# Kernel optimization log

Measured on AMD Instinct MI355X. Metric: run time of the kernel, lower is better.

## Reference

```python
import jax, jax.numpy as jnp
import numpy as np

H = 1024   # hidden_size
A = 16     # num_actions
T = 64     # time steps
N = 128    # batch (parallel envs)


def setup_inputs() -> dict:
    key = jax.random.key(0)
    ks = jax.random.split(key, 16)
    s = 0.02  # small-ish init scale for weights
    a_idx = jax.random.randint(ks[5], (T, N), 0, A)
    return {
        "x": jax.random.normal(ks[0], (T * N, H), jnp.float32),
        "hxs_gru": jax.random.normal(ks[1], (N, H), jnp.float32),
        "hxs_p": jax.random.normal(ks[2], (N, 2 * H), jnp.float32),
        # masks are 0/1 episode-reset flags
        "masks": jax.random.bernoulli(ks[3], 0.95, (T * N, 1)).astype(jnp.float32),
        "prev_action_one_hot": jax.nn.one_hot(a_idx, A, dtype=jnp.float32),
        "w_ih": jax.random.normal(ks[6], (3 * H, H), jnp.float32) * s,
        "w_hh": jax.random.normal(ks[7], (3 * H, H), jnp.float32) * s,
        "b_ih": jnp.zeros((3 * H,), jnp.float32),
        "b_hh": jnp.zeros((3 * H,), jnp.float32),
        "p_w1": jax.random.normal(ks[8], (2 * H, 2 * H + A), jnp.float32) * s,
        "p_b1": jnp.zeros((2 * H,), jnp.float32),
        "p_w2": jax.random.normal(ks[9], (H, 2 * H), jnp.float32) * s,
        "p_b2": jnp.zeros((H,), jnp.float32),
        "mu_w": jax.random.normal(ks[10], (H, H), jnp.float32) * s,
        "mu_b": jnp.zeros((H,), jnp.float32),
        "lv_w": jax.random.normal(ks[11], (H, H), jnp.float32) * s,
        "lv_b": jnp.zeros((H,), jnp.float32),
    }


def reference(x, hxs_gru, hxs_p, masks, prev_action_one_hot,
              w_ih, w_hh, b_ih, b_hh,
              p_w1, p_b1, p_w2, p_b2,
              mu_w, mu_b, lv_w, lv_b):
    n = hxs_gru.shape[0]
    h_dim = hxs_gru.shape[1]
    t = x.shape[0] // n
    xT = x.reshape(t, n, h_dim)        # [T,N,H]
    mT = masks.reshape(t, n, 1)        # [T,N,1]

    # ---- _forward_gru: masked GRUCell recurrence over time ----
    def gru_step(h, inp):
        x_t, m_t = inp
        h0 = h * m_t                                  # per-step state reset
        gi = x_t @ w_ih.T + b_ih                      # [N,3H]
        gh = h0 @ w_hh.T + b_hh                       # [N,3H]
        ir, iz, inn = jnp.split(gi, 3, axis=1)
        hr, hz, hn = jnp.split(gh, 3, axis=1)
        r = jax.nn.sigmoid(ir + hr)
        z = jax.nn.sigmoid(iz + hz)
        nn_ = jnp.tanh(inn + r * hn)
        h_new = (1.0 - z) * nn_ + z * h0              # PyTorch GRUCell update
        return h_new, h_new

    gru_hxs, gru_acc = jax.lax.scan(gru_step, hxs_gru, (xT, mT))
    gru_acc = gru_acc.reshape(t * n, h_dim)

    # ---- _forward_p_gru: MLP recurrence with mask-gated state/action ----
    def p_step(h, inp):
        x_t, m_t, a_t = inp
        hidden = h * m_t + jnp.concatenate([x_t, x_t], axis=1) * (1.0 - m_t)
        cur = jnp.concatenate([a_t * m_t, hidden], axis=1)   # [N, A+2H]
        d = jax.nn.relu(cur @ p_w1.T + p_b1)                 # [N, 2H]
        d = jax.nn.relu(d @ p_w2.T + p_b2)                   # [N, H]
        mu = d @ mu_w.T + mu_b                               # [N, H]
        lv = d @ lv_w.T + lv_b                               # [N, H]
        h_new = jnp.concatenate([mu, x_t], axis=1)           # [N, 2H]
        return h_new, (mu, lv)

    # note: original concatenates action first: cat((a*m, hidden))
    p_hxs, (p_mu, p_lv) = jax.lax.scan(p_step, hxs_p, (xT, mT, prev_action_one_hot))
    p_mu = p_mu.reshape(t * n, h_dim)
    p_lv = p_lv.reshape(t * n, h_dim)
    return (gru_acc, gru_hxs, p_mu, p_lv, p_hxs)
```

## Files before the change

kernel.cpp:

```cpp
#include <hip/hip_runtime.h>

typedef unsigned int uint;
typedef unsigned short ushort;
typedef __bf16 bf16x8_t __attribute__((ext_vector_type(8)));
typedef float f32x4_t __attribute__((ext_vector_type(4)));

__device__ __forceinline__ ushort f2b(float f) {
    uint u = __builtin_bit_cast(uint, f);
    u += 0x7fffu + ((u >> 16) & 1u);
    return (ushort)(u >> 16);
}
__device__ __forceinline__ float b2f(ushort h) {
    return __builtin_bit_cast(float, (uint)h << 16);
}
__device__ __forceinline__ float sigm(float v) { return 1.f / (1.f + __expf(-v)); }
__device__ __forceinline__ float tanh_(float v) {
    v = fmaxf(-15.f, fminf(15.f, v));
    float e = __expf(2.f * v);
    return (e - 1.f) / (e + 1.f);
}

__device__ __forceinline__ uint ld_cg_u32(const uint* p) {
    uint r;
    asm volatile("global_load_dword %0, %1, off sc0 sc1\n\ts_waitcnt vmcnt(0)"
                 : "=v"(r) : "v"(p) : "memory");
    return r;
}
__device__ __forceinline__ void st_cg_u32(uint* p, uint v) {
    asm volatile("global_store_dword %0, %1, off sc0 sc1" :: "v"(p), "v"(v) : "memory");
}
__device__ __forceinline__ void st_cg_u16(ushort* p, uint v) {
    asm volatile("global_store_short %0, %1, off sc0 sc1" :: "v"(p), "v"(v) : "memory");
}
__device__ __forceinline__ void ld8_nw(uint4 u[8],
    const void* p0, const void* p1, const void* p2, const void* p3,
    const void* p4, const void* p5, const void* p6, const void* p7)
{
    asm volatile(
        "global_load_dwordx4 %0, %8, off sc0 sc1\n\t"
        "global_load_dwordx4 %1, %9, off sc0 sc1\n\t"
        "global_load_dwordx4 %2, %10, off sc0 sc1\n\t"
        "global_load_dwordx4 %3, %11, off sc0 sc1\n\t"
        "global_load_dwordx4 %4, %12, off sc0 sc1\n\t"
        "global_load_dwordx4 %5, %13, off sc0 sc1\n\t"
        "global_load_dwordx4 %6, %14, off sc0 sc1\n\t"
        "global_load_dwordx4 %7, %15, off sc0 sc1"
        : "=&v"(u[0]), "=&v"(u[1]), "=&v"(u[2]), "=&v"(u[3]),
          "=&v"(u[4]), "=&v"(u[5]), "=&v"(u[6]), "=&v"(u[7])
        : "v"(p0), "v"(p1), "v"(p2), "v"(p3), "v"(p4), "v"(p5), "v"(p6), "v"(p7)
        : "memory");
}
__device__ __forceinline__ void vm0() {
    asm volatile("s_waitcnt vmcnt(0)" ::: "memory");
    __builtin_amdgcn_sched_barrier(0);
}
__device__ __forceinline__ bf16x8_t u2b(uint4 u) { return __builtin_bit_cast(bf16x8_t, u); }

#define SMEM_BYTES 36864
union U8 { ushort h[8]; uint4 v; };

template<int BN, int EPI, bool AF32>
__device__ __forceinline__ void gemm_body(
    int bx, int by, const void* Av, int lda,
    const ushort* Bp, int ldb, int K,
    void* Ov, int ldo, const float* bias, char* smem)
{
    constexpr int LDW = 72;
    ushort* As = (ushort*)smem;
    ushort* Bs = (ushort*)(smem + 128 * LDW * 2);
    const int tid = threadIdx.x, lane = tid & 63, wid = tid >> 6;
    constexpr int WC = (BN == 128) ? 2 : 1;
    constexpr int WR = 4 / WC;
    constexpr int WROWS = 128 / WR;
    constexpr int WCOLS = BN / WC;
    constexpr int MI = WROWS / 16, NI = WCOLS / 16;
    const int wr = (WC == 2) ? (wid >> 1) : wid;
    const int wc = (WC == 2) ? (wid & 1) : 0;
    const int row0 = by * 128, col0 = bx * BN;

    f32x4_t acc[MI][NI];
#pragma unroll
    for (int i = 0; i < MI; i++)
#pragma unroll
        for (int j = 0; j < NI; j++) acc[i][j] = (f32x4_t){0.f, 0.f, 0.f, 0.f};

    for (int k0 = 0; k0 < K; k0 += 64) {
        __syncthreads();
#pragma unroll
        for (int cc = 0; cc < 4; cc++) {
            int chunk = tid + cc * 256;
            int r = chunk >> 3, c8 = chunk & 7;
            uint4 val;
            if constexpr (AF32) {
                const float* Af = (const float*)Av + (size_t)(row0 + r) * lda + k0 + c8 * 8;
                float4 v0 = ((const float4*)Af)[0];
                float4 v1 = ((const float4*)Af)[1];
                U8 u;
                u.h[0] = f2b(v0.x); u.h[1] = f2b(v0.y); u.h[2] = f2b(v0.z); u.h[3] = f2b(v0.w);
                u.h[4] = f2b(v1.x); u.h[5] = f2b(v1.y); u.h[6] = f2b(v1.z); u.h[7] = f2b(v1.w);
                val = u.v;
            } else {
                val = *(const uint4*)((const ushort*)Av + (size_t)(row0 + r) * lda + k0 + c8 * 8);
            }
            *(uint4*)&As[r * LDW + c8 * 8] = val;
        }
#pragma unroll
        for (int cc = 0; cc < BN / 32; cc++) {
            int chunk = tid + cc * 256;
            int r = chunk >> 3, c8 = chunk & 7;
            uint4 val = *(const uint4*)(Bp + (size_t)(col0 + r) * ldb + k0 + c8 * 8);
            *(uint4*)&Bs[r * LDW + c8 * 8] = val;
        }
        __syncthreads();
#pragma unroll
        for (int kk = 0; kk < 64; kk += 32) {
            int ko = kk + ((lane >> 4) << 3);
            bf16x8_t af[MI], bf[NI];
#pragma unroll
            for (int mi = 0; mi < MI; mi++)
                af[mi] = *(const bf16x8_t*)&As[(wr * WROWS + mi * 16 + (lane & 15)) * LDW + ko];
#pragma unroll
            for (int ni = 0; ni < NI; ni++)
                bf[ni] = *(const bf16x8_t*)&Bs[(wc * WCOLS + ni * 16 + (lane & 15)) * LDW + ko];
#pragma unroll
            for (int mi = 0; mi < MI; mi++)
#pragma unroll
                for (int ni = 0; ni < NI; ni++)
                    acc[mi][ni] = __builtin_amdgcn_mfma_f32_16x16x32_bf16(af[mi], bf[ni], acc[mi][ni], 0, 0, 0);
        }
    }
#pragma unroll
    for (int mi = 0; mi < MI; mi++) {
#pragma unroll
        for (int ni = 0; ni < NI; ni++) {
            int gcol = col0 + wc * WCOLS + ni * 16 + (lane & 15);
#pragma unroll
            for (int i = 0; i < 4; i++) {
                int grow = row0 + wr * WROWS + mi * 16 + ((lane >> 4) << 2) + i;
                float v = acc[mi][ni][i];
                if constexpr (EPI == 0) {
                    ((float*)Ov)[(size_t)grow * ldo + gcol] = v + bias[gcol];
                } else if constexpr (EPI == 1) {
                    ((ushort*)Ov)[(size_t)grow * ldo + gcol] = f2b(v);
                } else {
                    ((ushort*)Ov)[(size_t)grow * ldo + gcol] = f2b(v + bias[gcol]);
                }
            }
        }
    }
}

template<int BN, int EPI, bool AF32>
__global__ __launch_bounds__(256) void gemm_k(
    const void* A, int lda, const ushort* B, int ldb, int K,
    void* O, int ldo, const float* bias)
{
    __shared__ char smem[SMEM_BYTES];
    gemm_body<BN, EPI, AF32>(blockIdx.x, blockIdx.y, A, lda, B, ldb, K, O, ldo, bias, smem);
}

#define NFLAG_G 0
#define NFLAG_A 4096
#define NFLAG_B 12288
#define NFLAGS  20480

__device__ __forceinline__ void wg_wait(uint* f, int n, int tid) {
    if (tid < n) {
        while (ld_cg_u32(f + tid) == 0u) __builtin_amdgcn_s_sleep(1);
    }
    __syncthreads();
}

__device__ __forceinline__ void wg_arrive(uint* slot, int tid) {
    __syncthreads();
    if (tid == 0) st_cg_u32(slot, 1u);
}

__device__ void role_gru(int cb, const ushort* __restrict__ whhb, ushort* hb,
                         const ushort* __restrict__ gi, const float* masks,
                         const float* b_ih, const float* b_hh, const float* hxs_g,
                         float* out, uint* flags, char* lds)
{
    const int tid = threadIdx.x, lane = tid & 63, w = tid >> 6;
    const int colL = cb * 16 + (lane & 15);
    const int kw = w * 256;
    const int kl = (lane >> 4) << 3;

    bf16x8_t bw[3][8];
#pragma unroll
    for (int g = 0; g < 3; g++)
#pragma unroll
        for (int ks = 0; ks < 8; ks++)
            bw[g][ks] = *(const bf16x8_t*)(whhb + (size_t)(g * 1024 + colL) * 1024 + kw + ks * 32 + kl);

    const float bihr = b_ih[colL], bihz = b_ih[1024 + colL], bihn = b_ih[2048 + colL];
    const float bhhr = b_hh[colL], bhhz = b_hh[1024 + colL], bhhn = b_hh[2048 + colL];

    f32x4_t hown[2];
#pragma unroll
    for (int j = 0; j < 2; j++)
#pragma unroll
        for (int i = 0; i < 4; i++)
            hown[j][i] = hxs_g[(size_t)((2 * w + j) * 16 + ((lane >> 4) << 2) + i) * 1024 + colL];

    for (int t = 0; t < 64; t++) {
        if (t) wg_wait(flags + NFLAG_G + (t - 1) * 64, 64, tid);
        float mc[2][4], mn[2][4], g0p[2][4], g1p[2][4], g2p[2][4];
#pragma unroll
        for (int j = 0; j < 2; j++) {
            const int rt = 2 * w + j;
#pragma unroll
            for (int i = 0; i < 4; i++) {
                const int row = rt * 16 + ((lane >> 4) << 2) + i;
                mc[j][i] = masks[t * 128 + row];
                mn[j][i] = (t < 63) ? masks[(t + 1) * 128 + row] : 0.f;
                const size_t gib = (size_t)(t * 128 + row) * 3072;
                g0p[j][i] = b2f(gi[gib + colL]);
                g1p[j][i] = b2f(gi[gib + 1024 + colL]);
                g2p[j][i] = b2f(gi[gib + 2048 + colL]);
            }
        }
        const ushort* A = hb + (size_t)(t & 1) * 131072;
        const ushort* base = A + (size_t)(lane & 15) * 1024 + kw + kl;
        f32x4_t acc[3][8];
#pragma unroll
        for (int g = 0; g < 3; g++)
#pragma unroll
            for (int rt = 0; rt < 8; rt++) acc[g][rt] = (f32x4_t){0.f, 0.f, 0.f, 0.f};
#pragma unroll
        for (int half = 0; half < 2; half++) {
            const ushort* b = base + half * 128;
            uint4 u0[8], u1[8], u2[8], u3[8];
            ld8_nw(u0, b, b + 16384, b + 32768, b + 49152, b + 65536, b + 81920, b + 98304, b + 114688);
            ld8_nw(u1, b + 32, b + 16384 + 32, b + 32768 + 32, b + 49152 + 32, b + 65536 + 32, b + 81920 + 32, b + 98304 + 32, b + 114688 + 32);
            ld8_nw(u2, b + 64, b + 16384 + 64, b + 32768 + 64, b + 49152 + 64, b + 65536 + 64, b + 81920 + 64, b + 98304 + 64, b + 114688 + 64);
            ld8_nw(u3, b + 96, b + 16384 + 96, b + 32768 + 96, b + 49152 + 96, b + 65536 + 96, b + 81920 + 96, b + 98304 + 96, b + 114688 + 96);
            vm0();
#pragma unroll
            for (int g = 0; g < 3; g++)
#pragma unroll
                for (int rt = 0; rt < 8; rt++) {
                    acc[g][rt] = __builtin_amdgcn_mfma_f32_16x16x32_bf16(u2b(u0[rt]), bw[g][half * 4 + 0], acc[g][rt], 0, 0, 0);
                    acc[g][rt] = __builtin_amdgcn_mfma_f32_16x16x32_bf16(u2b(u1[rt]), bw[g][half * 4 + 1], acc[g][rt], 0, 0, 0);
                    acc[g][rt] = __builtin_amdgcn_mfma_f32_16x16x32_bf16(u2b(u2[rt]), bw[g][half * 4 + 2], acc[g][rt], 0, 0, 0);
                    acc[g][rt] = __builtin_amdgcn_mfma_f32_16x16x32_bf16(u2b(u3[rt]), bw[g][half * 4 + 3], acc[g][rt], 0, 0, 0);
                }
        }
#pragma unroll
        for (int g = 0; g < 3; g++)
#pragma unroll
            for (int rt = 0; rt < 8; rt++)
                *(f32x4_t*)(lds + ((size_t)(w * 24 + g * 8 + rt) * 64 + lane) * 16) = acc[g][rt];
        __syncthreads();
#pragma unroll
        for (int j = 0; j < 2; j++) {
            const int rt = 2 * w + j;
            f32x4_t sg[3];
#pragma unroll
            for (int g = 0; g < 3; g++) {
                sg[g] = (f32x4_t){0.f, 0.f, 0.f, 0.f};
#pragma unroll
                for (int ww = 0; ww < 4; ww++)
                    sg[g] += *(const f32x4_t*)(lds + ((size_t)(ww * 24 + g * 8 + rt) * 64 + lane) * 16);
            }
#pragma unroll
            for (int i = 0; i < 4; i++) {
                const int row = rt * 16 + ((lane >> 4) << 2) + i;
                const float h0 = hown[j][i] * mc[j][i];
                const float rv = sigm(g0p[j][i] + bihr + bhhr + sg[0][i]);
                const float zv = sigm(g1p[j][i] + bihz + bhhz + sg[1][i]);
                const float nv = tanh_(g2p[j][i] + bihn + rv * (sg[2][i] + bhhn));
                const float hnew = (1.f - zv) * nv + zv * h0;
                out[(size_t)(t * 128 + row) * 1024 + colL] = hnew;
                hown[j][i] = hnew;
                if (t < 63)
                    st_cg_u16(hb + (size_t)((t + 1) & 1) * 131072 + (size_t)row * 1024 + colL,
                              (uint)f2b(hnew * mn[j][i]));
            }
        }
        wg_arrive(flags + NFLAG_G + t * 64 + cb, tid);
    }
}

__device__ void role_p(int p, const ushort* __restrict__ Wcb, const ushort* __restrict__ w1h1b,
                       const ushort* __restrict__ hp1b, const ushort* __restrict__ w2b,
                       const ushort* __restrict__ d1pre, const float* masks, const float* cvec,
                       const float* p_b2, ushort* d1r, ushort* d2r, uint* flags, char* lds)
{
    const int tid = threadIdx.x, lane = tid & 63, w = tid >> 6;
    const int rowg = p >> 6, colg = p & 63;
    const int rA0 = rowg * 64, cA0 = colg * 32;
    const int rB0 = rowg * 64, cB0 = colg * 16;
    const int kwA = w * 256, kwB = w * 512, kl = (lane >> 4) << 3;

    bf16x8_t wcF[2][8];
#pragma unroll
    for (int ct = 0; ct < 2; ct++)
#pragma unroll
        for (int ks = 0; ks < 8; ks++)
            wcF[ct][ks] = *(const bf16x8_t*)(Wcb + (size_t)(cA0 + ct * 16 + (lane & 15)) * 1024 + kwA + ks * 32 + kl);
    bf16x8_t w2F[16];
#pragma unroll
    for (int ks = 0; ks < 16; ks++)
        w2F[ks] = *(const bf16x8_t*)(w2b + (size_t)(cB0 + (lane & 15)) * 2048 + kwB + ks * 32 + kl);
    const float cv0 = cvec[cA0 + (lane & 15)], cv1 = cvec[cA0 + 16 + (lane & 15)];
    const float pb = p_b2[cB0 + (lane & 15)];

    for (int t = 0; t < 64; t++) {
        if (t) wg_wait(flags + NFLAG_B + (t - 1) * 128 + rowg * 64, 64, tid);
        float mA[4], preA[2][4];
#pragma unroll
        for (int i = 0; i < 4; i++) {
            const int row = rA0 + w * 16 + ((lane >> 4) << 2) + i;
            mA[i] = masks[t * 128 + row];
            preA[0][i] = b2f(d1pre[(size_t)(t * 128 + row) * 2048 + cA0 + (lane & 15)]);
            preA[1][i] = b2f(d1pre[(size_t)(t * 128 + row) * 2048 + cA0 + 16 + (lane & 15)]);
        }
        f32x4_t accA[2][4];
#pragma unroll
        for (int ct = 0; ct < 2; ct++)
#pragma unroll
            for (int rt = 0; rt < 4; rt++) accA[ct][rt] = (f32x4_t){0.f, 0.f, 0.f, 0.f};
        if (t == 0) {
#pragma unroll
            for (int ks = 0; ks < 8; ks++) {
                bf16x8_t af[4], b0[2];
#pragma unroll
                for (int ct = 0; ct < 2; ct++)
                    b0[ct] = *(const bf16x8_t*)(w1h1b + (size_t)(cA0 + ct * 16 + (lane & 15)) * 1024 + kwA + ks * 32 + kl);
#pragma unroll
                for (int rt = 0; rt < 4; rt++)
                    af[rt] = *(const bf16x8_t*)(hp1b + (size_t)(rA0 + rt * 16 + (lane & 15)) * 1024 + kwA + ks * 32 + kl);
#pragma unroll
                for (int ct = 0; ct < 2; ct++)
#pragma unroll
                    for (int rt = 0; rt < 4; rt++)
                        accA[ct][rt] = __builtin_amdgcn_mfma_f32_16x16x32_bf16(af[rt], b0[ct], accA[ct][rt], 0, 0, 0);
            }
        } else {
            const ushort* Ab = d2r + (size_t)(t - 1) * 131072 + (size_t)(rA0 + (lane & 15)) * 1024 + kwA + kl;
            uint4 u0[8], u1[8], u2[8], u3[8];
            ld8_nw(u0, Ab,       Ab + 16384,       Ab + 32768,       Ab + 49152,       Ab + 32,  Ab + 16384 + 32,  Ab + 32768 + 32,  Ab + 49152 + 32);
            ld8_nw(u1, Ab + 64,  Ab + 16384 + 64,  Ab + 32768 + 64,  Ab + 49152 + 64,  Ab + 96,  Ab + 16384 + 96,  Ab + 32768 + 96,  Ab + 49152 + 96);
            ld8_nw(u2, Ab + 128, Ab + 16384 + 128, Ab + 32768 + 128, Ab + 49152 + 128, Ab + 160, Ab + 16384 + 160, Ab + 32768 + 160, Ab + 49152 + 160);
            ld8_nw(u3, Ab + 192, Ab + 16384 + 192, Ab + 32768 + 192, Ab + 49152 + 192, Ab + 224, Ab + 16384 + 224, Ab + 32768 + 224, Ab + 49152 + 224);
            vm0();
#pragma unroll
            for (int ct = 0; ct < 2; ct++)
#pragma unroll
                for (int rt = 0; rt < 4; rt++) {
                    accA[ct][rt] = __builtin_amdgcn_mfma_f32_16x16x32_bf16(u2b(u0[rt]), wcF[ct][0], accA[ct][rt], 0, 0, 0);
                    accA[ct][rt] = __builtin_amdgcn_mfma_f32_16x16x32_bf16(u2b(u0[4 + rt]), wcF[ct][1], accA[ct][rt], 0, 0, 0);
                    accA[ct][rt] = __builtin_amdgcn_mfma_f32_16x16x32_bf16(u2b(u1[rt]), wcF[ct][2], accA[ct][rt], 0, 0, 0);
                    accA[ct][rt] = __builtin_amdgcn_mfma_f32_16x16x32_bf16(u2b(u1[4 + rt]), wcF[ct][3], accA[ct][rt], 0, 0, 0);
                    accA[ct][rt] = __builtin_amdgcn_mfma_f32_16x16x32_bf16(u2b(u2[rt]), wcF[ct][4], accA[ct][rt], 0, 0, 0);
                    accA[ct][rt] = __builtin_amdgcn_mfma_f32_16x16x32_bf16(u2b(u2[4 + rt]), wcF[ct][5], accA[ct][rt], 0, 0, 0);
                    accA[ct][rt] = __builtin_amdgcn_mfma_f32_16x16x32_bf16(u2b(u3[rt]), wcF[ct][6], accA[ct][rt], 0, 0, 0);
                    accA[ct][rt] = __builtin_amdgcn_mfma_f32_16x16x32_bf16(u2b(u3[4 + rt]), wcF[ct][7], accA[ct][rt], 0, 0, 0);
                }
        }
#pragma unroll
        for (int ct = 0; ct < 2; ct++)
#pragma unroll
            for (int rt = 0; rt < 4; rt++)
                *(f32x4_t*)(lds + ((size_t)(w * 8 + ct * 4 + rt) * 64 + lane) * 16) = accA[ct][rt];
        __syncthreads();
#pragma unroll
        for (int ct = 0; ct < 2; ct++) {
            f32x4_t s = (f32x4_t){0.f, 0.f, 0.f, 0.f};
#pragma unroll
            for (int ww = 0; ww < 4; ww++)
                s += *(const f32x4_t*)(lds + ((size_t)(ww * 8 + ct * 4 + w) * 64 + lane) * 16);
            const int col = cA0 + ct * 16 + (lane & 15);
            const float cvt = (t == 0) ? 0.f : (ct ? cv1 : cv0);
#pragma unroll
            for (int i = 0; i < 4; i++) {
                const int row = rA0 + w * 16 + ((lane >> 4) << 2) + i;
                float f = preA[ct][i] + mA[i] * (s[i] + cvt);
                st_cg_u16(d1r + (size_t)row * 2048 + col, (uint)f2b(f > 0.f ? f : 0.f));
            }
        }
        wg_arrive(flags + NFLAG_A + t * 128 + p, tid);
        wg_wait(flags + NFLAG_A + t * 128 + rowg * 64, 64, tid);
        f32x4_t accB[4];
#pragma unroll
        for (int rt = 0; rt < 4; rt++) accB[rt] = (f32x4_t){0.f, 0.f, 0.f, 0.f};
        const ushort* Bb = d1r + (size_t)(rB0 + (lane & 15)) * 2048 + kwB + kl;
#pragma unroll
        for (int half = 0; half < 2; half++) {
            const ushort* b = Bb + half * 256;
            uint4 u0[8], u1[8], u2[8], u3[8];
            ld8_nw(u0, b,       b + 32768,       b + 65536,       b + 98304,       b + 32,  b + 32768 + 32,  b + 65536 + 32,  b + 98304 + 32);
            ld8_nw(u1, b + 64,  b + 32768 + 64,  b + 65536 + 64,  b + 98304 + 64,  b + 96,  b + 32768 + 96,  b + 65536 + 96,  b + 98304 + 96);
            ld8_nw(u2, b + 128, b + 32768 + 128, b + 65536 + 128, b + 98304 + 128, b + 160, b + 32768 + 160, b + 65536 + 160, b + 98304 + 160);
            ld8_nw(u3, b + 192, b + 32768 + 192, b + 65536 + 192, b + 98304 + 192, b + 224, b + 32768 + 224, b + 65536 + 224, b + 98304 + 224);
            vm0();
#pragma unroll
            for (int rt = 0; rt < 4; rt++) {
                accB[rt] = __builtin_amdgcn_mfma_f32_16x16x32_bf16(u2b(u0[rt]), w2F[half * 8 + 0], accB[rt], 0, 0, 0);
                accB[rt] = __builtin_amdgcn_mfma_f32_16x16x32_bf16(u2b(u0[4 + rt]), w2F[half * 8 + 1], accB[rt], 0, 0, 0);
                accB[rt] = __builtin_amdgcn_mfma_f32_16x16x32_bf16(u2b(u1[rt]), w2F[half * 8 + 2], accB[rt], 0, 0, 0);
                accB[rt] = __builtin_amdgcn_mfma_f32_16x16x32_bf16(u2b(u1[4 + rt]), w2F[half * 8 + 3], accB[rt], 0, 0, 0);
                accB[rt] = __builtin_amdgcn_mfma_f32_16x16x32_bf16(u2b(u2[rt]), w2F[half * 8 + 4], accB[rt], 0, 0, 0);
                accB[rt] = __builtin_amdgcn_mfma_f32_16x16x32_bf16(u2b(u2[4 + rt]), w2F[half * 8 + 5], accB[rt], 0, 0, 0);
                accB[rt] = __builtin_amdgcn_mfma_f32_16x16x32_bf16(u2b(u3[rt]), w2F[half * 8 + 6], accB[rt], 0, 0, 0);
                accB[rt] = __builtin_amdgcn_mfma_f32_16x16x32_bf16(u2b(u3[4 + rt]), w2F[half * 8 + 7], accB[rt], 0, 0, 0);
            }
        }
#pragma unroll
        for (int rt = 0; rt < 4; rt++)
            *(f32x4_t*)(lds + ((size_t)(w * 4 + rt) * 64 + lane) * 16) = accB[rt];
        __syncthreads();
        {
            f32x4_t s = (f32x4_t){0.f, 0.f, 0.f, 0.f};
#pragma unroll
            for (int ww = 0; ww < 4; ww++)
                s += *(const f32x4_t*)(lds + ((size_t)(ww * 4 + w) * 64 + lane) * 16);
            const int col = cB0 + (lane & 15);
#pragma unroll
            for (int i = 0; i < 4; i++) {
                const int row = rB0 + w * 16 + ((lane >> 4) << 2) + i;
                float f = s[i] + pb;
                st_cg_u16(d2r + (size_t)(t * 128 + row) * 1024 + col, (uint)f2b(f > 0.f ? f : 0.f));
            }
        }
        wg_arrive(flags + NFLAG_B + t * 128 + p, tid);
    }
}

__global__ __launch_bounds__(256, 1) void persist_k(
    const ushort* whhb, const ushort* Wcb, const ushort* w1h1b, const ushort* w2b,
    const ushort* gi, const ushort* d1pre, const ushort* hp1b,
    ushort* hb, ushort* d1r, ushort* d2r,
    const float* masks, const float* b_ih, const float* b_hh,
    const float* cvec, const float* p_b2, const float* hxs_g,
    float* out, uint* flags)
{
    __shared__ __align__(16) char lds[98304];
    const int wg = blockIdx.x;
    if (wg < 64) role_gru(wg, whhb, hb, gi, masks, b_ih, b_hh, hxs_g, out, flags, lds);
    else         role_p(wg - 64, Wcb, w1h1b, hp1b, w2b, d1pre, masks, cvec, p_b2, d1r, d2r, flags, lds);
}

__global__ void prep_w(const float* w_ih, const float* w_hh, const float* p_w1,
                       const float* p_w2, const float* mu_w, const float* lv_w,
                       ushort* wihb, ushort* whhb, ushort* w2b, ushort* muwb,
                       ushort* lvwb, ushort* muwTb, ushort* w1h1b, ushort* pw1b)
{
    const long total = 17956864;
    for (long idx = (long)blockIdx.x * 256 + threadIdx.x; idx < total; idx += (long)gridDim.x * 256) {
        long l = idx;
        if (l < 3145728) { wihb[l] = f2b(w_ih[l]); continue; } l -= 3145728;
        if (l < 3145728) { whhb[l] = f2b(w_hh[l]); continue; } l -= 3145728;
        if (l < 2097152) { w2b[l] = f2b(p_w2[l]); continue; } l -= 2097152;
        if (l < 1048576) { muwb[l] = f2b(mu_w[l]); continue; } l -= 1048576;
        if (l < 1048576) { lvwb[l] = f2b(lv_w[l]); continue; } l -= 1048576;
        if (l < 1048576) {
            int c = (int)(l >> 10), o = (int)(l & 1023);
            muwTb[l] = f2b(mu_w[(size_t)o * 1024 + c]); continue;
        } l -= 1048576;
        if (l < 2097152) {
            int r = (int)(l >> 10), c = (int)(l & 1023);
            w1h1b[l] = f2b(p_w1[(size_t)r * 2064 + 16 + c]); continue;
        } l -= 2097152;
        {
            int r = (int)(l / 2112), c = (int)(l - (long)r * 2112);
            pw1b[l] = (c < 2064) ? f2b(p_w1[(size_t)r * 2064 + c]) : (ushort)0;
        }
    }
}

__global__ void prep_x(const float* x, const float* hxs_g, const float* hxs_p,
                       const float* masks, const float* oh,
                       ushort* ain, ushort* hb0, ushort* hp1b)
{
    const long totA = 8192L * 2112, totH = 131072, totP = 131072;
    for (long idx = (long)blockIdx.x * 256 + threadIdx.x; idx < totA + totH + totP; idx += (long)gridDim.x * 256) {
        if (idx < totA) {
            long j = idx;
            int i = (int)(j / 2112);
            int c = (int)(j - (long)i * 2112);
            float m = masks[i];
            float v;
            if (c < 16) v = oh[(size_t)i * 16 + c] * m;
            else if (c < 1040) v = x[(size_t)i * 1024 + (c - 16)] * (1.f - m);
            else if (c < 2064) {
                int cc = c - 1040;
                float xp = (i >= 128) ? x[(size_t)(i - 128) * 1024 + cc]
                                      : hxs_p[(size_t)i * 2048 + 1024 + cc];
                v = xp * m + x[(size_t)i * 1024 + cc] * (1.f - m);
            } else v = 0.f;
            ain[j] = f2b(v);
            continue;
        }
        long j = idx - totA;
        if (j < totH) {
            int row = (int)(j >> 10), c = (int)(j & 1023);
            hb0[j] = f2b(hxs_g[(size_t)row * 1024 + c] * masks[row]);
            continue;
        }
        j -= totH;
        {
            int row = (int)(j >> 10), c = (int)(j & 1023);
            hp1b[j] = f2b(hxs_p[(size_t)row * 2048 + c]);
        }
    }
}

__global__ void k_cvec(const float* p_w1, const float* mu_b, float* cvec)
{
    int j = blockIdx.x * 4 + (threadIdx.x >> 6);
    int lane = threadIdx.x & 63;
    float s = 0.f;
    for (int o = lane; o < 1024; o += 64) s += p_w1[(size_t)j * 2064 + 16 + o] * mu_b[o];
#pragma unroll
    for (int off = 32; off; off >>= 1) s += __shfl_down(s, off);
    if (lane == 0) cvec[j] = s;
}

__global__ void init_flags(uint* flags)
{
    int i = blockIdx.x * 256 + threadIdx.x;
    if (i < NFLAGS) flags[i] = 0u;
}

__global__ void k_tail(float* out, const float* x)
{
    const long total = 131072 + 262144;
    for (long idx = (long)blockIdx.x * 256 + threadIdx.x; idx < total; idx += (long)gridDim.x * 256) {
        if (idx < 131072) {
            out[8388608 + idx] = out[8257536 + idx];
        } else {
            long j = idx - 131072;
            int n = (int)(j >> 11), c = (int)(j & 2047);
            out[25296896 + j] = (c < 1024)
                ? out[8519680 + (size_t)(8064 + n) * 1024 + c]
                : x[(size_t)(8064 + n) * 1024 + (c - 1024)];
        }
    }
}

extern "C" void kernel_launch(void* const* d_in, const int* in_sizes, int n_in,
                              void* d_out, int out_size, void* d_ws, size_t ws_size,
                              hipStream_t stream)
{
    (void)in_sizes; (void)n_in; (void)out_size; (void)ws_size;
    const float* x      = (const float*)d_in[0];
    const float* hxs_g  = (const float*)d_in[1];
    const float* hxs_p  = (const float*)d_in[2];
    const float* masks  = (const float*)d_in[3];
    const float* oh     = (const float*)d_in[4];
    const float* w_ih   = (const float*)d_in[5];
    const float* w_hh   = (const float*)d_in[6];
    const float* b_ih   = (const float*)d_in[7];
    const float* b_hh   = (const float*)d_in[8];
    const float* p_w1   = (const float*)d_in[9];
    const float* p_b1   = (const float*)d_in[10];
    const float* p_w2   = (const float*)d_in[11];
    const float* p_b2   = (const float*)d_in[12];
    const float* mu_w   = (const float*)d_in[13];
    const float* mu_b   = (const float*)d_in[14];
    const float* lv_w   = (const float*)d_in[15];
    const float* lv_b   = (const float*)d_in[16];
    float* out = (float*)d_out;

    char* w = (char*)d_ws;
    ushort* gi     = (ushort*)(w + 0);
    ushort* ain    = (ushort*)(w + 0);
    ushort* d1pre  = (ushort*)(w + 50331648);
    ushort* wihb   = (ushort*)(w + 83886080);
    ushort* whhb   = (ushort*)(w + 90177536);
    ushort* pw1b   = (ushort*)(w + 96468992);
    ushort* w1h1b  = (ushort*)(w + 105119744);
    ushort* w2b    = (ushort*)(w + 109314048);
    ushort* muwb   = (ushort*)(w + 113508352);
    ushort* muwTb  = (ushort*)(w + 115605504);
    ushort* lvwb   = (ushort*)(w + 117702656);
    ushort* Wcb    = (ushort*)(w + 119799808);
    ushort* hp1b   = (ushort*)(w + 123994112);
    ushort* hb     = (ushort*)(w + 124256256);
    ushort* d1r    = (ushort*)(w + 124780544);
    ushort* d2r    = (ushort*)(w + 125304832);
    float*  cvec   = (float*) (w + 142082048);
    uint*   flags  = (uint*)  (w + 142090240);

    prep_w<<<dim3(2048), 256, 0, stream>>>(w_ih, w_hh, p_w1, p_w2, mu_w, lv_w,
                                           wihb, whhb, w2b, muwb, lvwb, muwTb, w1h1b, pw1b);
    prep_x<<<dim3(4096), 256, 0, stream>>>(x, hxs_g, hxs_p, masks, oh, ain, hb, hp1b);
    k_cvec<<<dim3(512), 256, 0, stream>>>(p_w1, mu_b, cvec);
    init_flags<<<dim3(80), 256, 0, stream>>>(flags);

    gemm_k<128, 2, false><<<dim3(16, 64), 256, 0, stream>>>(
        ain, 2112, pw1b, 2112, 2112, d1pre, 2048, p_b1);
    gemm_k<128, 1, true><<<dim3(24, 64), 256, 0, stream>>>(
        x, 1024, wihb, 1024, 1024, gi, 3072, nullptr);
    gemm_k<128, 1, false><<<dim3(8, 16), 256, 0, stream>>>(
        w1h1b, 1024, muwTb, 1024, 1024, Wcb, 1024, nullptr);

    persist_k<<<dim3(192), 256, 0, stream>>>(
        whhb, Wcb, w1h1b, w2b, gi, d1pre, hp1b, hb, d1r, d2r,
        masks, b_ih, b_hh, cvec, p_b2, hxs_g, out, flags);

    gemm_k<128, 0, false><<<dim3(8, 64), 256, 0, stream>>>(
        d2r, 1024, muwb, 1024, 1024, out + 8519680, 1024, mu_b);
    gemm_k<128, 0, false><<<dim3(8, 64), 256, 0, stream>>>(
        d2r, 1024, lvwb, 1024, 1024, out + 16908288, 1024, lv_b);

    k_tail<<<dim3(1536), 256, 0, stream>>>(out, x);
}
```

Before: 1.590 ms.

## Tile gi/d1pre layouts, per-step buffers, non-coherent loads, staged vector stores

The input-projection GEMMs now write gi and d1pre in a per-timestep, per-column-block tiled layout, so each persistent workgroup reads a contiguous block. Those reads are issued before the inter-workgroup flag wait, so they overlap the wait. The hidden-state buffer and the d1r/d2r buffers become one slot per timestep instead of a reused ping-pong buffer. This lets the recurrent loads drop the sc0/sc1 cache-bypass bits, since no slot is ever rewritten. Output tiles of the P role are staged in LDS and written with 16-byte stores instead of scattered 2-byte stores, at the cost of extra barriers and a much larger workspace.

```diff
diff --git a/kernel.cpp b/kernel.cpp
--- a/kernel.cpp
+++ b/kernel.cpp
@@ -4,6 +4,7 @@
 typedef unsigned short ushort;
 typedef __bf16 bf16x8_t __attribute__((ext_vector_type(8)));
 typedef float f32x4_t __attribute__((ext_vector_type(4)));
+typedef uint u32x4_t __attribute__((ext_vector_type(4)));
 
 __device__ __forceinline__ ushort f2b(float f) {
     uint u = __builtin_bit_cast(uint, f);
@@ -32,19 +33,22 @@
 __device__ __forceinline__ void st_cg_u16(ushort* p, uint v) {
     asm volatile("global_store_short %0, %1, off sc0 sc1" :: "v"(p), "v"(v) : "memory");
 }
-__device__ __forceinline__ void ld8_nw(uint4 u[8],
+__device__ __forceinline__ void st_cg_x4(ushort* p, u32x4_t v) {
+    asm volatile("global_store_dwordx4 %0, %1, off sc0 sc1" :: "v"(p), "v"(v) : "memory");
+}
+__device__ __forceinline__ void ld8_nc(uint4 u[8],
     const void* p0, const void* p1, const void* p2, const void* p3,
     const void* p4, const void* p5, const void* p6, const void* p7)
 {
     asm volatile(
-        "global_load_dwordx4 %0, %8, off sc0 sc1\n\t"
-        "global_load_dwordx4 %1, %9, off sc0 sc1\n\t"
-        "global_load_dwordx4 %2, %10, off sc0 sc1\n\t"
-        "global_load_dwordx4 %3, %11, off sc0 sc1\n\t"
-        "global_load_dwordx4 %4, %12, off sc0 sc1\n\t"
-        "global_load_dwordx4 %5, %13, off sc0 sc1\n\t"
-        "global_load_dwordx4 %6, %14, off sc0 sc1\n\t"
-        "global_load_dwordx4 %7, %15, off sc0 sc1"
+        "global_load_dwordx4 %0, %8, off\n\t"
+        "global_load_dwordx4 %1, %9, off\n\t"
+        "global_load_dwordx4 %2, %10, off\n\t"
+        "global_load_dwordx4 %3, %11, off\n\t"
+        "global_load_dwordx4 %4, %12, off\n\t"
+        "global_load_dwordx4 %5, %13, off\n\t"
+        "global_load_dwordx4 %6, %14, off\n\t"
+        "global_load_dwordx4 %7, %15, off"
         : "=&v"(u[0]), "=&v"(u[1]), "=&v"(u[2]), "=&v"(u[3]),
           "=&v"(u[4]), "=&v"(u[5]), "=&v"(u[6]), "=&v"(u[7])
         : "v"(p0), "v"(p1), "v"(p2), "v"(p3), "v"(p4), "v"(p5), "v"(p6), "v"(p7)
@@ -142,8 +146,16 @@
                     ((float*)Ov)[(size_t)grow * ldo + gcol] = v + bias[gcol];
                 } else if constexpr (EPI == 1) {
                     ((ushort*)Ov)[(size_t)grow * ldo + gcol] = f2b(v);
+                } else if constexpr (EPI == 2) {
+                    ((ushort*)Ov)[(size_t)grow * ldo + gcol] = f2b(v + bias[gcol]);
+                } else if constexpr (EPI == 3) {
+                    int t = grow >> 7, row = grow & 127;
+                    int g = gcol >> 10, cb = (gcol & 1023) >> 4, c16 = gcol & 15;
+                    ((ushort*)Ov)[(((size_t)t * 3 + g) * 64 + cb) * 2048 + row * 16 + c16] = f2b(v);
                 } else {
-                    ((ushort*)Ov)[(size_t)grow * ldo + gcol] = f2b(v + bias[gcol]);
+                    int t = grow >> 7, row = grow & 127;
+                    int cg = gcol >> 5, c32 = gcol & 31;
+                    ((ushort*)Ov)[((size_t)t * 64 + cg) * 4096 + row * 32 + c32] = f2b(v + bias[gcol]);
                 }
             }
         }
@@ -170,7 +182,6 @@
     }
     __syncthreads();
 }
-
 __device__ __forceinline__ void wg_arrive(uint* slot, int tid) {
     __syncthreads();
     if (tid == 0) st_cg_u32(slot, 1u);
@@ -204,8 +215,8 @@
             hown[j][i] = hxs_g[(size_t)((2 * w + j) * 16 + ((lane >> 4) << 2) + i) * 1024 + colL];
 
     for (int t = 0; t < 64; t++) {
-        if (t) wg_wait(flags + NFLAG_G + (t - 1) * 64, 64, tid);
         float mc[2][4], mn[2][4], g0p[2][4], g1p[2][4], g2p[2][4];
+        const size_t gb = ((size_t)t * 3 * 64 + cb) * 2048;
 #pragma unroll
         for (int j = 0; j < 2; j++) {
             const int rt = 2 * w + j;
@@ -214,14 +225,13 @@
                 const int row = rt * 16 + ((lane >> 4) << 2) + i;
                 mc[j][i] = masks[t * 128 + row];
                 mn[j][i] = (t < 63) ? masks[(t + 1) * 128 + row] : 0.f;
-                const size_t gib = (size_t)(t * 128 + row) * 3072;
-                g0p[j][i] = b2f(gi[gib + colL]);
-                g1p[j][i] = b2f(gi[gib + 1024 + colL]);
-                g2p[j][i] = b2f(gi[gib + 2048 + colL]);
-            }
-        }
-        const ushort* A = hb + (size_t)(t & 1) * 131072;
-        const ushort* base = A + (size_t)(lane & 15) * 1024 + kw + kl;
+                g0p[j][i] = b2f(gi[gb + row * 16 + (lane & 15)]);
+                g1p[j][i] = b2f(gi[gb + 131072 + row * 16 + (lane & 15)]);
+                g2p[j][i] = b2f(gi[gb + 262144 + row * 16 + (lane & 15)]);
+            }
+        }
+        if (t) wg_wait(flags + NFLAG_G + (t - 1) * 64, 64, tid);
+        const ushort* base = hb + (size_t)t * 131072 + (size_t)(lane & 15) * 1024 + kw + kl;
         f32x4_t acc[3][8];
 #pragma unroll
         for (int g = 0; g < 3; g++)
@@ -231,10 +241,10 @@
         for (int half = 0; half < 2; half++) {
             const ushort* b = base + half * 128;
             uint4 u0[8], u1[8], u2[8], u3[8];
-            ld8_nw(u0, b, b + 16384, b + 32768, b + 49152, b + 65536, b + 81920, b + 98304, b + 114688);
-            ld8_nw(u1, b + 32, b + 16384 + 32, b + 32768 + 32, b + 49152 + 32, b + 65536 + 32, b + 81920 + 32, b + 98304 + 32, b + 114688 + 32);
-            ld8_nw(u2, b + 64, b + 16384 + 64, b + 32768 + 64, b + 49152 + 64, b + 65536 + 64, b + 81920 + 64, b + 98304 + 64, b + 114688 + 64);
-            ld8_nw(u3, b + 96, b + 16384 + 96, b + 32768 + 96, b + 49152 + 96, b + 65536 + 96, b + 81920 + 96, b + 98304 + 96, b + 114688 + 96);
+            ld8_nc(u0, b, b + 16384, b + 32768, b + 49152, b + 65536, b + 81920, b + 98304, b + 114688);
+            ld8_nc(u1, b + 32, b + 16384 + 32, b + 32768 + 32, b + 49152 + 32, b + 65536 + 32, b + 81920 + 32, b + 98304 + 32, b + 114688 + 32);
+            ld8_nc(u2, b + 64, b + 16384 + 64, b + 32768 + 64, b + 49152 + 64, b + 65536 + 64, b + 81920 + 64, b + 98304 + 64, b + 114688 + 64);
+            ld8_nc(u3, b + 96, b + 16384 + 96, b + 32768 + 96, b + 49152 + 96, b + 65536 + 96, b + 81920 + 96, b + 98304 + 96, b + 114688 + 96);
             vm0();
 #pragma unroll
             for (int g = 0; g < 3; g++)
@@ -274,7 +284,7 @@
                 out[(size_t)(t * 128 + row) * 1024 + colL] = hnew;
                 hown[j][i] = hnew;
                 if (t < 63)
-                    st_cg_u16(hb + (size_t)((t + 1) & 1) * 131072 + (size_t)row * 1024 + colL,
+                    st_cg_u16(hb + (size_t)(t + 1) * 131072 + (size_t)row * 1024 + colL,
                               (uint)f2b(hnew * mn[j][i]));
             }
         }
@@ -292,6 +302,7 @@
     const int rA0 = rowg * 64, cA0 = colg * 32;
     const int rB0 = rowg * 64, cB0 = colg * 16;
     const int kwA = w * 256, kwB = w * 512, kl = (lane >> 4) << 3;
+    ushort* stg = (ushort*)(lds + 32768) + w * 512;
 
     bf16x8_t wcF[2][8];
 #pragma unroll
@@ -307,15 +318,16 @@
     const float pb = p_b2[cB0 + (lane & 15)];
 
     for (int t = 0; t < 64; t++) {
-        if (t) wg_wait(flags + NFLAG_B + (t - 1) * 128 + rowg * 64, 64, tid);
         float mA[4], preA[2][4];
+        const size_t pbase = ((size_t)t * 64 + colg) * 4096;
 #pragma unroll
         for (int i = 0; i < 4; i++) {
             const int row = rA0 + w * 16 + ((lane >> 4) << 2) + i;
             mA[i] = masks[t * 128 + row];
-            preA[0][i] = b2f(d1pre[(size_t)(t * 128 + row) * 2048 + cA0 + (lane & 15)]);
-            preA[1][i] = b2f(d1pre[(size_t)(t * 128 + row) * 2048 + cA0 + 16 + (lane & 15)]);
-        }
+            preA[0][i] = b2f(d1pre[pbase + (row & 127) * 32 + (lane & 15)]);
+            preA[1][i] = b2f(d1pre[pbase + (row & 127) * 32 + 16 + (lane & 15)]);
+        }
+        if (t) wg_wait(flags + NFLAG_B + (t - 1) * 128 + rowg * 64, 64, tid);
         f32x4_t accA[2][4];
 #pragma unroll
         for (int ct = 0; ct < 2; ct++)
@@ -340,10 +352,10 @@
         } else {
             const ushort* Ab = d2r + (size_t)(t - 1) * 131072 + (size_t)(rA0 + (lane & 15)) * 1024 + kwA + kl;
             uint4 u0[8], u1[8], u2[8], u3[8];
-            ld8_nw(u0, Ab,       Ab + 16384,       Ab + 32768,       Ab + 49152,       Ab + 32,  Ab + 16384 + 32,  Ab + 32768 + 32,  Ab + 49152 + 32);
-            ld8_nw(u1, Ab + 64,  Ab + 16384 + 64,  Ab + 32768 + 64,  Ab + 49152 + 64,  Ab + 96,  Ab + 16384 + 96,  Ab + 32768 + 96,  Ab + 49152 + 96);
-            ld8_nw(u2, Ab + 128, Ab + 16384 + 128, Ab + 32768 + 128, Ab + 49152 + 128, Ab + 160, Ab + 16384 + 160, Ab + 32768 + 160, Ab + 49152 + 160);
-            ld8_nw(u3, Ab + 192, Ab + 16384 + 192, Ab + 32768 + 192, Ab + 49152 + 192, Ab + 224, Ab + 16384 + 224, Ab + 32768 + 224, Ab + 49152 + 224);
+            ld8_nc(u0, Ab,       Ab + 16384,       Ab + 32768,       Ab + 49152,       Ab + 32,  Ab + 16384 + 32,  Ab + 32768 + 32,  Ab + 49152 + 32);
+            ld8_nc(u1, Ab + 64,  Ab + 16384 + 64,  Ab + 32768 + 64,  Ab + 49152 + 64,  Ab + 96,  Ab + 16384 + 96,  Ab + 32768 + 96,  Ab + 49152 + 96);
+            ld8_nc(u2, Ab + 128, Ab + 16384 + 128, Ab + 32768 + 128, Ab + 49152 + 128, Ab + 160, Ab + 16384 + 160, Ab + 32768 + 160, Ab + 49152 + 160);
+            ld8_nc(u3, Ab + 192, Ab + 16384 + 192, Ab + 32768 + 192, Ab + 49152 + 192, Ab + 224, Ab + 16384 + 224, Ab + 32768 + 224, Ab + 49152 + 224);
             vm0();
 #pragma unroll
             for (int ct = 0; ct < 2; ct++)
@@ -359,6 +371,7 @@
                     accA[ct][rt] = __builtin_amdgcn_mfma_f32_16x16x32_bf16(u2b(u3[4 + rt]), wcF[ct][7], accA[ct][rt], 0, 0, 0);
                 }
         }
+        __syncthreads();
 #pragma unroll
         for (int ct = 0; ct < 2; ct++)
 #pragma unroll
@@ -371,29 +384,33 @@
 #pragma unroll
             for (int ww = 0; ww < 4; ww++)
                 s += *(const f32x4_t*)(lds + ((size_t)(ww * 8 + ct * 4 + w) * 64 + lane) * 16);
-            const int col = cA0 + ct * 16 + (lane & 15);
             const float cvt = (t == 0) ? 0.f : (ct ? cv1 : cv0);
 #pragma unroll
             for (int i = 0; i < 4; i++) {
-                const int row = rA0 + w * 16 + ((lane >> 4) << 2) + i;
                 float f = preA[ct][i] + mA[i] * (s[i] + cvt);
-                st_cg_u16(d1r + (size_t)row * 2048 + col, (uint)f2b(f > 0.f ? f : 0.f));
-            }
+                stg[(((lane >> 4) << 2) + i) * 32 + ct * 16 + (lane & 15)] = f2b(f > 0.f ? f : 0.f);
+            }
+        }
+        __syncthreads();
+        {
+            const int rl = lane >> 2, c8 = (lane & 3) * 8;
+            u32x4_t v = *(const u32x4_t*)&stg[rl * 32 + c8];
+            st_cg_x4(d1r + (size_t)t * 262144 + (size_t)(rA0 + w * 16 + rl) * 2048 + cA0 + c8, v);
         }
         wg_arrive(flags + NFLAG_A + t * 128 + p, tid);
         wg_wait(flags + NFLAG_A + t * 128 + rowg * 64, 64, tid);
         f32x4_t accB[4];
 #pragma unroll
         for (int rt = 0; rt < 4; rt++) accB[rt] = (f32x4_t){0.f, 0.f, 0.f, 0.f};
-        const ushort* Bb = d1r + (size_t)(rB0 + (lane & 15)) * 2048 + kwB + kl;
+        const ushort* Bb = d1r + (size_t)t * 262144 + (size_t)(rB0 + (lane & 15)) * 2048 + kwB + kl;
 #pragma unroll
         for (int half = 0; half < 2; half++) {
             const ushort* b = Bb + half * 256;
             uint4 u0[8], u1[8], u2[8], u3[8];
-            ld8_nw(u0, b,       b + 32768,       b + 65536,       b + 98304,       b + 32,  b + 32768 + 32,  b + 65536 + 32,  b + 98304 + 32);
-            ld8_nw(u1, b + 64,  b + 32768 + 64,  b + 65536 + 64,  b + 98304 + 64,  b + 96,  b + 32768 + 96,  b + 65536 + 96,  b + 98304 + 96);
-            ld8_nw(u2, b + 128, b + 32768 + 128, b + 65536 + 128, b + 98304 + 128, b + 160, b + 32768 + 160, b + 65536 + 160, b + 98304 + 160);
-            ld8_nw(u3, b + 192, b + 32768 + 192, b + 65536 + 192, b + 98304 + 192, b + 224, b + 32768 + 224, b + 65536 + 224, b + 98304 + 224);
+            ld8_nc(u0, b,       b + 32768,       b + 65536,       b + 98304,       b + 32,  b + 32768 + 32,  b + 65536 + 32,  b + 98304 + 32);
+            ld8_nc(u1, b + 64,  b + 32768 + 64,  b + 65536 + 64,  b + 98304 + 64,  b + 96,  b + 32768 + 96,  b + 65536 + 96,  b + 98304 + 96);
+            ld8_nc(u2, b + 128, b + 32768 + 128, b + 65536 + 128, b + 98304 + 128, b + 160, b + 32768 + 160, b + 65536 + 160, b + 98304 + 160);
+            ld8_nc(u3, b + 192, b + 32768 + 192, b + 65536 + 192, b + 98304 + 192, b + 224, b + 32768 + 224, b + 65536 + 224, b + 98304 + 224);
             vm0();
 #pragma unroll
             for (int rt = 0; rt < 4; rt++) {
@@ -407,6 +424,7 @@
                 accB[rt] = __builtin_amdgcn_mfma_f32_16x16x32_bf16(u2b(u3[4 + rt]), w2F[half * 8 + 7], accB[rt], 0, 0, 0);
             }
         }
+        __syncthreads();
 #pragma unroll
         for (int rt = 0; rt < 4; rt++)
             *(f32x4_t*)(lds + ((size_t)(w * 4 + rt) * 64 + lane) * 16) = accB[rt];
@@ -416,12 +434,18 @@
 #pragma unroll
             for (int ww = 0; ww < 4; ww++)
                 s += *(const f32x4_t*)(lds + ((size_t)(ww * 4 + w) * 64 + lane) * 16);
-            const int col = cB0 + (lane & 15);
 #pragma unroll
             for (int i = 0; i < 4; i++) {
-                const int row = rB0 + w * 16 + ((lane >> 4) << 2) + i;
                 float f = s[i] + pb;
-                st_cg_u16(d2r + (size_t)(t * 128 + row) * 1024 + col, (uint)f2b(f > 0.f ? f : 0.f));
+                stg[(((lane >> 4) << 2) + i) * 16 + (lane & 15)] = f2b(f > 0.f ? f : 0.f);
+            }
+        }
+        __syncthreads();
+        {
+            if (lane < 32) {
+                const int rl = lane >> 1, c8 = (lane & 1) * 8;
+                u32x4_t v = *(const u32x4_t*)&stg[rl * 16 + c8];
+                st_cg_x4(d2r + (size_t)t * 131072 + (size_t)(rB0 + w * 16 + rl) * 1024 + cB0 + c8, v);
             }
         }
         wg_arrive(flags + NFLAG_B + t * 128 + p, tid);
@@ -579,10 +603,10 @@
     ushort* Wcb    = (ushort*)(w + 119799808);
     ushort* hp1b   = (ushort*)(w + 123994112);
     ushort* hb     = (ushort*)(w + 124256256);
-    ushort* d1r    = (ushort*)(w + 124780544);
-    ushort* d2r    = (ushort*)(w + 125304832);
-    float*  cvec   = (float*) (w + 142082048);
-    uint*   flags  = (uint*)  (w + 142090240);
+    ushort* d1r    = (ushort*)(w + 141033472);
+    ushort* d2r    = (ushort*)(w + 174587904);
+    float*  cvec   = (float*) (w + 191365120);
+    uint*   flags  = (uint*)  (w + 191373312);
 
     prep_w<<<dim3(2048), 256, 0, stream>>>(w_ih, w_hh, p_w1, p_w2, mu_w, lv_w,
                                            wihb, whhb, w2b, muwb, lvwb, muwTb, w1h1b, pw1b);
@@ -590,10 +614,10 @@
     k_cvec<<<dim3(512), 256, 0, stream>>>(p_w1, mu_b, cvec);
     init_flags<<<dim3(80), 256, 0, stream>>>(flags);
 
-    gemm_k<128, 2, false><<<dim3(16, 64), 256, 0, stream>>>(
-        ain, 2112, pw1b, 2112, 2112, d1pre, 2048, p_b1);
-    gemm_k<128, 1, true><<<dim3(24, 64), 256, 0, stream>>>(
-        x, 1024, wihb, 1024, 1024, gi, 3072, nullptr);
+    gemm_k<128, 4, false><<<dim3(16, 64), 256, 0, stream>>>(
+        ain, 2112, pw1b, 2112, 2112, d1pre, 0, p_b1);
+    gemm_k<128, 3, true><<<dim3(24, 64), 256, 0, stream>>>(
+        x, 1024, wihb, 1024, 1024, gi, 0, nullptr);
     gemm_k<128, 1, false><<<dim3(8, 16), 256, 0, stream>>>(
         w1h1b, 1024, muwTb, 1024, 1024, Wcb, 1024, nullptr);
 
```

Measured after the change: 1.410 ms. -11.3%, faster.
